# Kernel optimization log

Measured on AMD Instinct MI355X. Metric: run time of the kernel, lower is better.

## Reference

```python
import jax, jax.numpy as jnp
import numpy as np

D_MODEL = 1024
NUM_HEADS = 16
D_K = D_MODEL // NUM_HEADS


def setup_inputs() -> dict:
    key = jax.random.key(0)
    ks = jax.random.split(key, 11)
    B, S = 2, 2048
    scale = 1.0 / np.sqrt(D_MODEL)
    inp = {
        "Q": jax.random.normal(ks[0], (B, S, D_MODEL), jnp.float32),
        "K": jax.random.normal(ks[1], (B, S, D_MODEL), jnp.float32),
        "V": jax.random.normal(ks[2], (B, S, D_MODEL), jnp.float32),
        "W_q": jax.random.normal(ks[3], (D_MODEL, D_MODEL), jnp.float32) * scale,
        "b_q": jnp.zeros((D_MODEL,), jnp.float32),
        "W_k": jax.random.normal(ks[4], (D_MODEL, D_MODEL), jnp.float32) * scale,
        "b_k": jnp.zeros((D_MODEL,), jnp.float32),
        "W_v": jax.random.normal(ks[5], (D_MODEL, D_MODEL), jnp.float32) * scale,
        "b_v": jnp.zeros((D_MODEL,), jnp.float32),
        "W_o": jax.random.normal(ks[6], (D_MODEL, D_MODEL), jnp.float32) * scale,
        "b_o": jnp.zeros((D_MODEL,), jnp.float32),
    }
    return inp


def _split_heads(x):
    # [B, S, D] -> [B, H, S, d_k]
    B, S, _ = x.shape
    return x.reshape(B, S, NUM_HEADS, D_K).transpose(0, 2, 1, 3)


def reference(Q, K, V, W_q, b_q, W_k, b_k, W_v, b_v, W_o, b_o):
    # linear projections (torch Linear: x @ W.T + b)
    q = _split_heads(Q @ W_q.T + b_q)
    k = _split_heads(K @ W_k.T + b_k)
    v = _split_heads(V @ W_v.T + b_v)
    # scaled dot-product attention, full [B,H,S,S] scores as in source
    scores = jnp.einsum("bhqd,bhkd->bhqk", q, k) / jnp.sqrt(jnp.float32(D_K))
    probs = jax.nn.softmax(scores, axis=-1)
    ctx = jnp.einsum("bhqk,bhkd->bhqd", probs, v)
    # combine heads: [B,H,S,d_k] -> [B,S,D]
    B, H, S, d = ctx.shape
    ctx = ctx.transpose(0, 2, 1, 3).reshape(B, S, H * d)
    return ctx @ W_o.T + b_o
```

## Files before the change

kernel.cpp:

```cpp
#include <hip/hip_runtime.h>
#include <hip/hip_bf16.h>

typedef unsigned short u16;
typedef unsigned int u32;
typedef short s16x8 __attribute__((ext_vector_type(8)));
typedef float f32x4 __attribute__((ext_vector_type(4)));
typedef float f32x16 __attribute__((ext_vector_type(16)));
typedef u32 u32x4 __attribute__((ext_vector_type(4)));

#define DEV static __device__ __forceinline__

DEV u16 bf16_rne(float f) {
  u32 u = __builtin_bit_cast(u32, f);
  u += 0x7fffu + ((u >> 16) & 1u);
  return (u16)(u >> 16);
}

DEV u32 pack2_bf16(float a, float b) {
  u32 ua = __builtin_bit_cast(u32, a);
  u32 ub = __builtin_bit_cast(u32, b);
  ua += 0x7fffu + ((ua >> 16) & 1u);
  ub += 0x7fffu + ((ub >> 16) & 1u);
  return (ua >> 16) | (ub & 0xffff0000u);
}

#define GLDS16(g, l)                                                           \
  __builtin_amdgcn_global_load_lds(                                           \
      (const __attribute__((address_space(1))) void*)(g),                     \
      (__attribute__((address_space(3))) void*)(l), 16, 0, 0)

__global__ void cvt4_kernel(const float* s0, const float* s1, const float* s2,
                            const float* s3, u16* d0, u16* d1, u16* d2,
                            u16* d3, int n4) {
  const int z = blockIdx.y;
  const float* s = (z == 0) ? s0 : (z == 1) ? s1 : (z == 2) ? s2 : s3;
  u16* d = (z == 0) ? d0 : (z == 1) ? d1 : (z == 2) ? d2 : d3;
  int i = blockIdx.x * blockDim.x + threadIdx.x;
  if (i < n4) {
    float4 v = reinterpret_cast<const float4*>(s)[i];
    ushort4 o;
    o.x = bf16_rne(v.x);
    o.y = bf16_rne(v.y);
    o.z = bf16_rne(v.z);
    o.w = bf16_rne(v.w);
    reinterpret_cast<ushort4*>(d)[i] = o;
  }
}

__global__ __launch_bounds__(256, 3) void gemm_qkv(
    const float* __restrict__ A0, const float* __restrict__ A1,
    const float* __restrict__ A2, const u16* __restrict__ W0,
    const u16* __restrict__ W1, const u16* __restrict__ W2,
    const float* __restrict__ bias0, const float* __restrict__ bias1,
    const float* __restrict__ bias2, u16* __restrict__ C0,
    u16* __restrict__ C1v, u16* __restrict__ C2, int M, int N, int K) {
  const int z = blockIdx.z;
  const float* A = (z == 0) ? A0 : (z == 1) ? A1 : A2;
  const u16* W = (z == 0) ? W0 : (z == 1) ? W1 : W2;
  const float* bias = (z == 0) ? bias0 : (z == 1) ? bias1 : bias2;
  u16* Cout = (z == 0) ? C0 : (z == 1) ? C1v : C2;
  const float escale = (z == 0) ? 0.125f * 1.44269504088896f : 1.0f;

  __shared__ __align__(16) u16 As[128 * 64];
  __shared__ __align__(16) u16 Ws[128 * 64];
  const int tid = threadIdx.x;
  const int lane = tid & 63;
  const int w = tid >> 6;
  const int wr = w >> 1, wc = w & 1;
  const int l15 = lane & 15, l4 = lane >> 4;
  const int m0 = blockIdx.x * 128, n0 = blockIdx.y * 128;

  f32x4 acc[4][4] = {};
  float bv[4];
#pragma unroll
  for (int fc = 0; fc < 4; ++fc) bv[fc] = bias[n0 + wc * 64 + fc * 16 + l15];

  float4 pre[4][2];
  auto loadA = [&](int kt) {
#pragma unroll
    for (int i = 0; i < 4; ++i) {
      const int ch = i * 256 + tid;
      const float* s = A + (size_t)(m0 + (ch >> 3)) * K + kt + (ch & 7) * 8;
      pre[i][0] = *(const float4*)s;
      pre[i][1] = *(const float4*)(s + 4);
    }
  };
  loadA(0);

  for (int kt = 0; kt < K; kt += 64) {
    __syncthreads();
#pragma unroll
    for (int i = 0; i < 4; ++i) {
      const int ch = i * 256 + tid;
      const int row = ch >> 3, cg = ch & 7;
      u32x4 o;
      o[0] = pack2_bf16(pre[i][0].x, pre[i][0].y);
      o[1] = pack2_bf16(pre[i][0].z, pre[i][0].w);
      o[2] = pack2_bf16(pre[i][1].x, pre[i][1].y);
      o[3] = pack2_bf16(pre[i][1].z, pre[i][1].w);
      *(u32x4*)(As + (size_t)(row * 8 + (cg ^ (row & 7))) * 8) = o;
    }
#pragma unroll
    for (int i = 0; i < 4; ++i) {
      const int ch = i * 256 + tid;
      const int row = ch >> 3, cl = ch & 7;
      GLDS16(W + (size_t)(n0 + row) * K + kt + ((cl ^ (row & 7)) * 8),
             Ws + (size_t)(i * 256 + w * 64) * 8);
    }
    __syncthreads();
    if (kt + 64 < K) loadA(kt + 64);
#pragma unroll
    for (int ks = 0; ks < 2; ++ks) {
      const int sw = (ks * 4 + l4) ^ (l15 & 7);
      s16x8 a[4], b[4];
#pragma unroll
      for (int f = 0; f < 4; ++f)
        a[f] = *(const s16x8*)(As + (size_t)((wr * 64 + f * 16 + l15) * 8 + sw) * 8);
#pragma unroll
      for (int f = 0; f < 4; ++f)
        b[f] = *(const s16x8*)(Ws + (size_t)((wc * 64 + f * 16 + l15) * 8 + sw) * 8);
#pragma unroll
      for (int fr = 0; fr < 4; ++fr)
#pragma unroll
        for (int fc = 0; fc < 4; ++fc)
          acc[fr][fc] = __builtin_amdgcn_mfma_f32_16x16x32_bf16(
              a[fr], b[fc], acc[fr][fc], 0, 0, 0);
    }
  }

  if (z == 2) {
#pragma unroll
    for (int fr = 0; fr < 4; ++fr) {
      const int m = m0 + wr * 64 + fr * 16 + l4 * 4;
      const int bb = m >> 11, s = m & 2047;
#pragma unroll
      for (int fc = 0; fc < 4; ++fc) {
        const int n = n0 + wc * 64 + fc * 16 + l15;
        const int hh = n >> 6, dd = n & 63;
        ushort4 o;
        o.x = bf16_rne(acc[fr][fc][0] + bv[fc]);
        o.y = bf16_rne(acc[fr][fc][1] + bv[fc]);
        o.z = bf16_rne(acc[fr][fc][2] + bv[fc]);
        o.w = bf16_rne(acc[fr][fc][3] + bv[fc]);
        *(ushort4*)(Cout + (((size_t)(bb * 16 + hh) * 64 + dd) * 2048 + s)) = o;
      }
    }
  } else {
#pragma unroll
    for (int fr = 0; fr < 4; ++fr) {
      const int mrow = m0 + wr * 64 + fr * 16 + l4 * 4;
#pragma unroll
      for (int fc = 0; fc < 4; ++fc) {
        const int ncol = n0 + wc * 64 + fc * 16 + l15;
#pragma unroll
        for (int r = 0; r < 4; ++r)
          Cout[(size_t)(mrow + r) * N + ncol] =
              bf16_rne((acc[fr][fc][r] + bv[fc]) * escale);
      }
    }
  }
}

__global__ __launch_bounds__(256, 4) void gemm_o(
    const u16* __restrict__ A, const u16* __restrict__ W,
    const float* __restrict__ bias, float* __restrict__ Cout, int M, int N,
    int K) {
  __shared__ __align__(16) u16 As[128 * 64];
  __shared__ __align__(16) u16 Ws[64 * 64];
  const int tid = threadIdx.x;
  const int lane = tid & 63;
  const int w = tid >> 6;
  const int wr = w >> 1, wc = w & 1;
  const int l15 = lane & 15, l4 = lane >> 4;
  const int m0 = blockIdx.x * 128, n0 = blockIdx.y * 64;

  f32x4 acc[4][2] = {};
  float bv[2];
#pragma unroll
  for (int fc = 0; fc < 2; ++fc) bv[fc] = bias[n0 + wc * 32 + fc * 16 + l15];

  for (int kt = 0; kt < K; kt += 64) {
    __syncthreads();
#pragma unroll
    for (int i = 0; i < 4; ++i) {
      const int ch = i * 256 + tid;
      const int row = ch >> 3, cl = ch & 7;
      GLDS16(A + (size_t)(m0 + row) * K + kt + ((cl ^ (row & 7)) * 8),
             As + (size_t)(i * 256 + w * 64) * 8);
    }
#pragma unroll
    for (int i = 0; i < 2; ++i) {
      const int ch = i * 256 + tid;
      const int row = ch >> 3, cl = ch & 7;
      GLDS16(W + (size_t)(n0 + row) * K + kt + ((cl ^ (row & 7)) * 8),
             Ws + (size_t)(i * 256 + w * 64) * 8);
    }
    __syncthreads();
#pragma unroll
    for (int ks = 0; ks < 2; ++ks) {
      const int sw = (ks * 4 + l4) ^ (l15 & 7);
      s16x8 a[4], b[2];
#pragma unroll
      for (int f = 0; f < 4; ++f)
        a[f] = *(const s16x8*)(As + (size_t)((wr * 64 + f * 16 + l15) * 8 + sw) * 8);
#pragma unroll
      for (int f = 0; f < 2; ++f)
        b[f] = *(const s16x8*)(Ws + (size_t)((wc * 32 + f * 16 + l15) * 8 + sw) * 8);
#pragma unroll
      for (int fr = 0; fr < 4; ++fr)
#pragma unroll
        for (int fc = 0; fc < 2; ++fc)
          acc[fr][fc] = __builtin_amdgcn_mfma_f32_16x16x32_bf16(
              a[fr], b[fc], acc[fr][fc], 0, 0, 0);
    }
  }

#pragma unroll
  for (int fr = 0; fr < 4; ++fr) {
    const int mrow = m0 + wr * 64 + fr * 16 + l4 * 4;
#pragma unroll
    for (int fc = 0; fc < 2; ++fc) {
      const int ncol = n0 + wc * 32 + fc * 16 + l15;
#pragma unroll
      for (int r = 0; r < 4; ++r)
        Cout[(size_t)(mrow + r) * N + ncol] = acc[fr][fc][r] + bv[fc];
    }
  }
}

__global__ __launch_bounds__(512, 4) void attn_fused(
    const u16* __restrict__ qp, const u16* __restrict__ kp,
    const u16* __restrict__ vt, u16* __restrict__ ctx) {
  const int S = 2048, D = 1024;
  const int bh = blockIdx.x;
  const int qt = blockIdx.y;
  const int tid = threadIdx.x, lane = tid & 63, w = tid >> 6;
  const int l31 = lane & 31, l5 = lane >> 5;
  const int g = tid >> 8;
  const int tl = tid & 255;
  const int wl = tl >> 6;
  const int wq = w & 3;

  __shared__ __align__(16) u16 SM[32768];

  const size_t qkbase = ((size_t)(bh >> 4) * S) * D + (size_t)(bh & 15) * 64;
  const size_t vbase = (size_t)bh * 64 * S;

  const int q = qt * 128 + wq * 32 + l31;
  s16x8 qf[4];
#pragma unroll
  for (int ks = 0; ks < 4; ++ks)
    qf[ks] = *(const s16x8*)(qp + qkbase + (size_t)q * D + ks * 16 + l5 * 8);

  u32x4 onesw;
  onesw[0] = onesw[1] = onesw[2] = onesw[3] = 0x3F803F80u;
  const s16x8 ones = __builtin_bit_cast(s16x8, onesw);

  f32x16 octx[2] = {};
  f32x16 lacc = {};

  auto stage = [&](int buf, int ti) {
    const int kv0 = (g * 16 + ti) * 64;
    u16* Kd = SM + g * 16384 + buf * 4096;
    u16* Vd = SM + g * 16384 + 8192 + buf * 4096;
#pragma unroll
    for (int i = 0; i < 2; ++i) {
      const int gch = i * 256 + tl;
      const int kv = gch >> 3, cc = gch & 7;
      GLDS16(kp + qkbase + (size_t)(kv0 + kv) * D + ((cc ^ (kv & 7)) << 3),
             Kd + (size_t)(i * 256 + wl * 64) * 8);
    }
#pragma unroll
    for (int i = 0; i < 2; ++i) {
      const int gch = i * 256 + tl;
      const int d = gch >> 3, cc = gch & 7;
      GLDS16(vt + vbase + (size_t)d * S + kv0 + ((cc ^ (d & 7)) << 3),
             Vd + (size_t)(i * 256 + wl * 64) * 8);
    }
  };

  stage(0, 0);
  const int NT = 16;
  for (int t = 0; t < NT; ++t) {
    __syncthreads();
    if (t + 1 < NT) stage((t + 1) & 1, t + 1);
    const u16* Kb = SM + g * 16384 + (t & 1) * 4096;
    const u16* Vb = SM + g * 16384 + 8192 + (t & 1) * 4096;

    f32x16 sc[2] = {};
#pragma unroll
    for (int ks = 0; ks < 4; ++ks) {
      __builtin_amdgcn_s_setprio(1);
#pragma unroll
      for (int fk = 0; fk < 2; ++fk) {
        const int kv = fk * 32 + l31;
        const int c = (ks << 1) + l5;
        const s16x8 kf =
            *(const s16x8*)(Kb + (size_t)(kv * 8 + (c ^ (kv & 7))) * 8);
        sc[fk] = __builtin_amdgcn_mfma_f32_32x32x16_bf16(kf, qf[ks], sc[fk],
                                                         0, 0, 0);
      }
      __builtin_amdgcn_s_setprio(0);
    }

#pragma unroll
    for (int c4 = 0; c4 < 4; ++c4) {
      const int fk = c4 >> 1, hf = c4 & 1;
      float p[8];
#pragma unroll
      for (int j = 0; j < 8; ++j)
        p[j] = __builtin_amdgcn_exp2f(sc[fk][hf * 8 + j]);
      u32 x0, x1, y0, y1;
      asm("v_cvt_pk_bf16_f32 %0, %1, %2" : "=v"(x0) : "v"(p[0]), "v"(p[1]));
      asm("v_cvt_pk_bf16_f32 %0, %1, %2" : "=v"(x1) : "v"(p[2]), "v"(p[3]));
      asm("v_cvt_pk_bf16_f32 %0, %1, %2" : "=v"(y0) : "v"(p[4]), "v"(p[5]));
      asm("v_cvt_pk_bf16_f32 %0, %1, %2" : "=v"(y1) : "v"(p[6]), "v"(p[7]));
      asm("v_permlane32_swap_b32 %0, %1" : "+v"(x0), "+v"(y0));
      asm("v_permlane32_swap_b32 %0, %1" : "+v"(x1), "+v"(y1));
      u32x4 bw;
      bw[0] = x0; bw[1] = x1; bw[2] = y0; bw[3] = y1;
      const s16x8 pb = __builtin_bit_cast(s16x8, bw);
      __builtin_amdgcn_s_setprio(1);
      lacc = __builtin_amdgcn_mfma_f32_32x32x16_bf16(ones, pb, lacc, 0, 0, 0);
#pragma unroll
      for (int fd = 0; fd < 2; ++fd) {
        const int d = fd * 32 + l31;
        const int c = (c4 << 1) + l5;
        const s16x8 vf =
            *(const s16x8*)(Vb + (size_t)(d * 8 + (c ^ (d & 7))) * 8);
        octx[fd] = __builtin_amdgcn_mfma_f32_32x32x16_bf16(vf, pb, octx[fd],
                                                           0, 0, 0);
      }
      __builtin_amdgcn_s_setprio(0);
    }
  }

  const float lpart = lacc[0];

  __syncthreads();
  float* scr = (float*)(void*)SM;
  if (g == 1) {
    float* dst = scr + ((size_t)wq * 64 + lane) * 33;
#pragma unroll
    for (int fd = 0; fd < 2; ++fd)
#pragma unroll
      for (int r = 0; r < 16; ++r) dst[fd * 16 + r] = octx[fd][r];
    dst[32] = lpart;
  }
  __syncthreads();
  if (g == 0) {
    const float* src = scr + ((size_t)wq * 64 + lane) * 33;
    const float linv = 1.f / (lpart + src[32]);
#pragma unroll
    for (int fd = 0; fd < 2; ++fd)
#pragma unroll
      for (int gg = 0; gg < 4; ++gg) {
        ushort4 o;
        o.x = bf16_rne((octx[fd][gg * 4 + 0] + src[fd * 16 + gg * 4 + 0]) * linv);
        o.y = bf16_rne((octx[fd][gg * 4 + 1] + src[fd * 16 + gg * 4 + 1]) * linv);
        o.z = bf16_rne((octx[fd][gg * 4 + 2] + src[fd * 16 + gg * 4 + 2]) * linv);
        o.w = bf16_rne((octx[fd][gg * 4 + 3] + src[fd * 16 + gg * 4 + 3]) * linv);
        *(ushort4*)(ctx + qkbase + (size_t)q * D + fd * 32 + gg * 8 + l5 * 4) =
            o;
      }
  }
}

extern "C" void kernel_launch(void* const* d_in, const int* in_sizes, int n_in,
                              void* d_out, int out_size, void* d_ws,
                              size_t ws_size, hipStream_t stream) {
  (void)in_sizes; (void)n_in; (void)out_size; (void)ws_size;
  const float* Q = (const float*)d_in[0];
  const float* K = (const float*)d_in[1];
  const float* V = (const float*)d_in[2];
  const float* Wq = (const float*)d_in[3];
  const float* bq = (const float*)d_in[4];
  const float* Wk = (const float*)d_in[5];
  const float* bk = (const float*)d_in[6];
  const float* Wv = (const float*)d_in[7];
  const float* bv = (const float*)d_in[8];
  const float* Wo = (const float*)d_in[9];
  const float* bo = (const float*)d_in[10];

  const int B = 2, S = 2048, D = 1024, H = 16;
  const int M = B * S;
  const size_t NE = (size_t)M * D;
  const size_t WE = (size_t)D * D;

  u16* qp = (u16*)d_ws;
  u16* kp = qp + NE;
  u16* vtb = kp + NE;
  u16* ctxb = vtb + NE;
  u16* Wqb = ctxb + NE;
  u16* Wkb = Wqb + WE;
  u16* Wvb = Wkb + WE;
  u16* Wob = Wvb + WE;

  const int w4 = (int)(WE / 4), wb = (w4 + 255) / 256;
  cvt4_kernel<<<dim3(wb, 4), 256, 0, stream>>>(Wq, Wk, Wv, Wo, Wqb, Wkb, Wvb,
                                               Wob, w4);

  dim3 gg(M / 128, D / 128, 3);
  gemm_qkv<<<gg, 256, 0, stream>>>(Q, K, V, Wqb, Wkb, Wvb, bq, bk, bv, qp, kp,
                                   vtb, M, D, D);

  dim3 ga(B * H, S / 128);
  attn_fused<<<ga, 512, 0, stream>>>(qp, kp, vtb, ctxb);

  dim3 go(M / 128, D / 64);
  gemm_o<<<go, 256, 0, stream>>>(ctxb, Wob, bo, (float*)d_out, M, D, D);
}
```

Before: 105.3 us.

## Software-pipeline QKV GEMM with double-buffered weight tiles and two-deep A prefetch

Restructures the QKV projection GEMM main loop into a software pipeline: weight tiles are double-buffered in LDS via direct global-to-LDS loads issued one step ahead, and fp32 activation tiles are prefetched two steps ahead into alternating register sets. It waits with explicit vmcnt/lgkmcnt counts and s_barrier plus sched_barrier fences instead of __syncthreads, and fully unrolls the K loop assuming K=1024. The goal is to hide global load latency behind MFMA work. In exchange it uses more LDS and registers, which may lower occupancy under launch_bounds(256,3), and it hardcodes K and the vmcnt value.

```diff
diff --git a/kernel.cpp b/kernel.cpp
--- a/kernel.cpp
+++ b/kernel.cpp
@@ -62,71 +62,100 @@
   const float escale = (z == 0) ? 0.125f * 1.44269504088896f : 1.0f;
 
   __shared__ __align__(16) u16 As[128 * 64];
-  __shared__ __align__(16) u16 Ws[128 * 64];
+  __shared__ __align__(16) u16 Ws[2][128 * 64];
   const int tid = threadIdx.x;
   const int lane = tid & 63;
   const int w = tid >> 6;
-  const int wr = w >> 1, wc = w & 1;
+  const int wr = w >> 1, wcol = w & 1;
   const int l15 = lane & 15, l4 = lane >> 4;
   const int m0 = blockIdx.x * 128, n0 = blockIdx.y * 128;
 
   f32x4 acc[4][4] = {};
   float bv[4];
 #pragma unroll
-  for (int fc = 0; fc < 4; ++fc) bv[fc] = bias[n0 + wc * 64 + fc * 16 + l15];
-
-  float4 pre[4][2];
-  auto loadA = [&](int kt) {
-#pragma unroll
-    for (int i = 0; i < 4; ++i) {
-      const int ch = i * 256 + tid;
-      const float* s = A + (size_t)(m0 + (ch >> 3)) * K + kt + (ch & 7) * 8;
-      pre[i][0] = *(const float4*)s;
-      pre[i][1] = *(const float4*)(s + 4);
-    }
-  };
-  loadA(0);
-
-  for (int kt = 0; kt < K; kt += 64) {
-    __syncthreads();
-#pragma unroll
-    for (int i = 0; i < 4; ++i) {
-      const int ch = i * 256 + tid;
-      const int row = ch >> 3, cg = ch & 7;
-      u32x4 o;
-      o[0] = pack2_bf16(pre[i][0].x, pre[i][0].y);
-      o[1] = pack2_bf16(pre[i][0].z, pre[i][0].w);
-      o[2] = pack2_bf16(pre[i][1].x, pre[i][1].y);
-      o[3] = pack2_bf16(pre[i][1].z, pre[i][1].w);
-      *(u32x4*)(As + (size_t)(row * 8 + (cg ^ (row & 7))) * 8) = o;
-    }
-#pragma unroll
-    for (int i = 0; i < 4; ++i) {
-      const int ch = i * 256 + tid;
-      const int row = ch >> 3, cl = ch & 7;
-      GLDS16(W + (size_t)(n0 + row) * K + kt + ((cl ^ (row & 7)) * 8),
-             Ws + (size_t)(i * 256 + w * 64) * 8);
-    }
-    __syncthreads();
-    if (kt + 64 < K) loadA(kt + 64);
-#pragma unroll
-    for (int ks = 0; ks < 2; ++ks) {
-      const int sw = (ks * 4 + l4) ^ (l15 & 7);
-      s16x8 a[4], b[4];
-#pragma unroll
-      for (int f = 0; f < 4; ++f)
-        a[f] = *(const s16x8*)(As + (size_t)((wr * 64 + f * 16 + l15) * 8 + sw) * 8);
-#pragma unroll
-      for (int f = 0; f < 4; ++f)
-        b[f] = *(const s16x8*)(Ws + (size_t)((wc * 64 + f * 16 + l15) * 8 + sw) * 8);
-#pragma unroll
-      for (int fr = 0; fr < 4; ++fr)
-#pragma unroll
-        for (int fc = 0; fc < 4; ++fc)
-          acc[fr][fc] = __builtin_amdgcn_mfma_f32_16x16x32_bf16(
-              a[fr], b[fc], acc[fr][fc], 0, 0, 0);
-    }
-  }
+  for (int fc = 0; fc < 4; ++fc) bv[fc] = bias[n0 + wcol * 64 + fc * 16 + l15];
+
+  float4 pA0[4][2], pA1[4][2];
+
+#define LOADA(kt, P)                                                           \
+  {                                                                            \
+    _Pragma("unroll") for (int i = 0; i < 4; ++i) {                            \
+      const int ch = i * 256 + tid;                                            \
+      const float* sA = A + (size_t)(m0 + (ch >> 3)) * K + (kt) + (ch & 7) * 8;\
+      P[i][0] = *(const float4*)sA;                                            \
+      P[i][1] = *(const float4*)(sA + 4);                                      \
+    }                                                                          \
+  }
+#define GLDSW(kt, bufi)                                                        \
+  {                                                                            \
+    _Pragma("unroll") for (int i = 0; i < 4; ++i) {                            \
+      const int ch = i * 256 + tid;                                            \
+      const int row = ch >> 3, cl = ch & 7;                                    \
+      GLDS16(W + (size_t)(n0 + row) * K + (kt) + ((cl ^ (row & 7)) * 8),       \
+             &Ws[bufi][(size_t)(i * 256 + w * 64) * 8]);                       \
+    }                                                                          \
+  }
+#define CVTA(P)                                                                \
+  {                                                                            \
+    _Pragma("unroll") for (int i = 0; i < 4; ++i) {                            \
+      const int ch = i * 256 + tid;                                            \
+      const int row = ch >> 3, cg = ch & 7;                                    \
+      u32x4 o;                                                                 \
+      o[0] = pack2_bf16(P[i][0].x, P[i][0].y);                                 \
+      o[1] = pack2_bf16(P[i][0].z, P[i][0].w);                                 \
+      o[2] = pack2_bf16(P[i][1].x, P[i][1].y);                                 \
+      o[3] = pack2_bf16(P[i][1].z, P[i][1].w);                                 \
+      *(u32x4*)(As + (size_t)(row * 8 + (cg ^ (row & 7))) * 8) = o;            \
+    }                                                                          \
+  }
+#define COMPUTE(bufi)                                                          \
+  {                                                                            \
+    _Pragma("unroll") for (int ks = 0; ks < 2; ++ks) {                         \
+      const int sw = (ks * 4 + l4) ^ (l15 & 7);                                \
+      s16x8 a[4], b[4];                                                        \
+      _Pragma("unroll") for (int f = 0; f < 4; ++f) a[f] =                     \
+          *(const s16x8*)(As + (size_t)((wr * 64 + f * 16 + l15) * 8 + sw) * 8);\
+      _Pragma("unroll") for (int f = 0; f < 4; ++f) b[f] =                     \
+          *(const s16x8*)(&Ws[bufi][0] +                                       \
+                          (size_t)((wcol * 64 + f * 16 + l15) * 8 + sw) * 8);  \
+      _Pragma("unroll") for (int fr = 0; fr < 4; ++fr)                         \
+          _Pragma("unroll") for (int fc = 0; fc < 4; ++fc) acc[fr][fc] =       \
+              __builtin_amdgcn_mfma_f32_16x16x32_bf16(a[fr], b[fc],            \
+                                                      acc[fr][fc], 0, 0, 0);   \
+    }                                                                          \
+  }
+
+  LOADA(0, pA0);
+  GLDSW(0, 0);
+  LOADA(64, pA1);
+  CVTA(pA0);
+
+#define ITER(t, WC, WN, PL, PC)                                                \
+  {                                                                            \
+    GLDSW((((t) + 1) & 15) * 64, WN);                                          \
+    LOADA((((t) + 2) & 15) * 64, PL);                                          \
+    asm volatile("s_waitcnt vmcnt(20)" ::: "memory");         \
+    __builtin_amdgcn_sched_barrier(0);                                         \
+    asm volatile("s_waitcnt lgkmcnt(0)" ::: "memory");     \
+    __builtin_amdgcn_sched_barrier(0);                                         \
+    __builtin_amdgcn_s_barrier();                   \
+    __builtin_amdgcn_sched_barrier(0);                                         \
+    COMPUTE(WC);                                                               \
+    __builtin_amdgcn_sched_barrier(0);                                         \
+    __builtin_amdgcn_s_barrier();                     \
+    __builtin_amdgcn_sched_barrier(0);                                         \
+    if ((t) < 15) CVTA(PC);                            \
+  }
+
+  for (int tt = 0; tt < 8; ++tt) {
+    ITER(2 * tt, 0, 1, pA0, pA1);
+    ITER(2 * tt + 1, 1, 0, pA1, pA0);
+  }
+#undef ITER
+#undef COMPUTE
+#undef CVTA
+#undef GLDSW
+#undef LOADA
 
   if (z == 2) {
 #pragma unroll
@@ -135,7 +164,7 @@
       const int bb = m >> 11, s = m & 2047;
 #pragma unroll
       for (int fc = 0; fc < 4; ++fc) {
-        const int n = n0 + wc * 64 + fc * 16 + l15;
+        const int n = n0 + wcol * 64 + fc * 16 + l15;
         const int hh = n >> 6, dd = n & 63;
         ushort4 o;
         o.x = bf16_rne(acc[fr][fc][0] + bv[fc]);
@@ -151,7 +180,7 @@
       const int mrow = m0 + wr * 64 + fr * 16 + l4 * 4;
 #pragma unroll
       for (int fc = 0; fc < 4; ++fc) {
-        const int ncol = n0 + wc * 64 + fc * 16 + l15;
+        const int ncol = n0 + wcol * 64 + fc * 16 + l15;
 #pragma unroll
         for (int r = 0; r < 4; ++r)
           Cout[(size_t)(mrow + r) * N + ncol] =
```

Result: slower. 128.1 us (+21.6%).

## Pre-convert Q/K/V inputs to bf16 and load A tiles via global_load_lds

Applied to the files above, without the earlier changes.

Adds a separate conversion pass that turns the fp32 Q, K and V activations into bf16 buffers. The QKV GEMM then streams A tiles directly into LDS with global_load_lds instead of loading fp32 into registers, packing and writing them. The GEMM tile is also narrowed from 128x128 to 128x64 with a higher occupancy bound, and the Q bf16 buffer is reused to hold the attention context. This removes register pressure and in-loop conversion work, at the cost of an extra kernel launch and an extra full read and write of the activations.

```diff
diff --git a/kernel.cpp b/kernel.cpp
--- a/kernel.cpp
+++ b/kernel.cpp
@@ -14,14 +14,6 @@
   u32 u = __builtin_bit_cast(u32, f);
   u += 0x7fffu + ((u >> 16) & 1u);
   return (u16)(u >> 16);
-}
-
-DEV u32 pack2_bf16(float a, float b) {
-  u32 ua = __builtin_bit_cast(u32, a);
-  u32 ub = __builtin_bit_cast(u32, b);
-  ua += 0x7fffu + ((ua >> 16) & 1u);
-  ub += 0x7fffu + ((ub >> 16) & 1u);
-  return (ua >> 16) | (ub & 0xffff0000u);
 }
 
 #define GLDS16(g, l)                                                           \
@@ -47,82 +39,65 @@
   }
 }
 
-__global__ __launch_bounds__(256, 3) void gemm_qkv(
-    const float* __restrict__ A0, const float* __restrict__ A1,
-    const float* __restrict__ A2, const u16* __restrict__ W0,
+__global__ __launch_bounds__(256, 5) void gemm_qkv(
+    const u16* __restrict__ A0, const u16* __restrict__ A1,
+    const u16* __restrict__ A2, const u16* __restrict__ W0,
     const u16* __restrict__ W1, const u16* __restrict__ W2,
     const float* __restrict__ bias0, const float* __restrict__ bias1,
     const float* __restrict__ bias2, u16* __restrict__ C0,
     u16* __restrict__ C1v, u16* __restrict__ C2, int M, int N, int K) {
   const int z = blockIdx.z;
-  const float* A = (z == 0) ? A0 : (z == 1) ? A1 : A2;
+  const u16* A = (z == 0) ? A0 : (z == 1) ? A1 : A2;
   const u16* W = (z == 0) ? W0 : (z == 1) ? W1 : W2;
   const float* bias = (z == 0) ? bias0 : (z == 1) ? bias1 : bias2;
   u16* Cout = (z == 0) ? C0 : (z == 1) ? C1v : C2;
   const float escale = (z == 0) ? 0.125f * 1.44269504088896f : 1.0f;
 
   __shared__ __align__(16) u16 As[128 * 64];
-  __shared__ __align__(16) u16 Ws[128 * 64];
+  __shared__ __align__(16) u16 Ws[64 * 64];
   const int tid = threadIdx.x;
   const int lane = tid & 63;
   const int w = tid >> 6;
   const int wr = w >> 1, wc = w & 1;
   const int l15 = lane & 15, l4 = lane >> 4;
-  const int m0 = blockIdx.x * 128, n0 = blockIdx.y * 128;
-
-  f32x4 acc[4][4] = {};
-  float bv[4];
-#pragma unroll
-  for (int fc = 0; fc < 4; ++fc) bv[fc] = bias[n0 + wc * 64 + fc * 16 + l15];
-
-  float4 pre[4][2];
-  auto loadA = [&](int kt) {
+  const int m0 = blockIdx.x * 128, n0 = blockIdx.y * 64;
+
+  f32x4 acc[4][2] = {};
+  float bv[2];
+#pragma unroll
+  for (int fc = 0; fc < 2; ++fc) bv[fc] = bias[n0 + wc * 32 + fc * 16 + l15];
+
+  for (int kt = 0; kt < K; kt += 64) {
+    __syncthreads();
 #pragma unroll
     for (int i = 0; i < 4; ++i) {
       const int ch = i * 256 + tid;
-      const float* s = A + (size_t)(m0 + (ch >> 3)) * K + kt + (ch & 7) * 8;
-      pre[i][0] = *(const float4*)s;
-      pre[i][1] = *(const float4*)(s + 4);
-    }
-  };
-  loadA(0);
-
-  for (int kt = 0; kt < K; kt += 64) {
-    __syncthreads();
-#pragma unroll
-    for (int i = 0; i < 4; ++i) {
-      const int ch = i * 256 + tid;
-      const int row = ch >> 3, cg = ch & 7;
-      u32x4 o;
-      o[0] = pack2_bf16(pre[i][0].x, pre[i][0].y);
-      o[1] = pack2_bf16(pre[i][0].z, pre[i][0].w);
-      o[2] = pack2_bf16(pre[i][1].x, pre[i][1].y);
-      o[3] = pack2_bf16(pre[i][1].z, pre[i][1].w);
-      *(u32x4*)(As + (size_t)(row * 8 + (cg ^ (row & 7))) * 8) = o;
-    }
-#pragma unroll
-    for (int i = 0; i < 4; ++i) {
+      const int row = ch >> 3, cl = ch & 7;
+      GLDS16(A + (size_t)(m0 + row) * K + kt + ((cl ^ (row & 7)) * 8),
+             As + (size_t)(i * 256 + w * 64) * 8);
+    }
+#pragma unroll
+    for (int i = 0; i < 2; ++i) {
       const int ch = i * 256 + tid;
       const int row = ch >> 3, cl = ch & 7;
       GLDS16(W + (size_t)(n0 + row) * K + kt + ((cl ^ (row & 7)) * 8),
              Ws + (size_t)(i * 256 + w * 64) * 8);
     }
     __syncthreads();
-    if (kt + 64 < K) loadA(kt + 64);
 #pragma unroll
     for (int ks = 0; ks < 2; ++ks) {
       const int sw = (ks * 4 + l4) ^ (l15 & 7);
-      s16x8 a[4], b[4];
+      s16x8 a[4], b[2];
 #pragma unroll
       for (int f = 0; f < 4; ++f)
         a[f] = *(const s16x8*)(As + (size_t)((wr * 64 + f * 16 + l15) * 8 + sw) * 8);
 #pragma unroll
-      for (int f = 0; f < 4; ++f)
-        b[f] = *(const s16x8*)(Ws + (size_t)((wc * 64 + f * 16 + l15) * 8 + sw) * 8);
+      for (int f = 0; f < 2; ++f)
+        b[f] = *(const s16x8*)(Ws + (size_t)((wc * 32 + f * 16 + l15) * 8 + sw) * 8);
 #pragma unroll
       for (int fr = 0; fr < 4; ++fr)
 #pragma unroll
-        for (int fc = 0; fc < 4; ++fc)
+        for (int fc = 0; fc < 2; ++fc)
           acc[fr][fc] = __builtin_amdgcn_mfma_f32_16x16x32_bf16(
               a[fr], b[fc], acc[fr][fc], 0, 0, 0);
     }
@@ -134,8 +109,8 @@
       const int m = m0 + wr * 64 + fr * 16 + l4 * 4;
       const int bb = m >> 11, s = m & 2047;
 #pragma unroll
-      for (int fc = 0; fc < 4; ++fc) {
-        const int n = n0 + wc * 64 + fc * 16 + l15;
+      for (int fc = 0; fc < 2; ++fc) {
+        const int n = n0 + wc * 32 + fc * 16 + l15;
         const int hh = n >> 6, dd = n & 63;
         ushort4 o;
         o.x = bf16_rne(acc[fr][fc][0] + bv[fc]);
@@ -150,8 +125,8 @@
     for (int fr = 0; fr < 4; ++fr) {
       const int mrow = m0 + wr * 64 + fr * 16 + l4 * 4;
 #pragma unroll
-      for (int fc = 0; fc < 4; ++fc) {
-        const int ncol = n0 + wc * 64 + fc * 16 + l15;
+      for (int fc = 0; fc < 2; ++fc) {
+        const int ncol = n0 + wc * 32 + fc * 16 + l15;
 #pragma unroll
         for (int r = 0; r < 4; ++r)
           Cout[(size_t)(mrow + r) * N + ncol] =
@@ -387,26 +362,31 @@
   const size_t NE = (size_t)M * D;
   const size_t WE = (size_t)D * D;
 
-  u16* qp = (u16*)d_ws;
+  u16* Qb = (u16*)d_ws;
+  u16* Kb = Qb + NE;
+  u16* Vb = Kb + NE;
+  u16* qp = Vb + NE;
   u16* kp = qp + NE;
   u16* vtb = kp + NE;
-  u16* ctxb = vtb + NE;
-  u16* Wqb = ctxb + NE;
+  u16* Wqb = vtb + NE;
   u16* Wkb = Wqb + WE;
   u16* Wvb = Wkb + WE;
   u16* Wob = Wvb + WE;
 
+  const int n4 = (int)(NE / 4), nb = (n4 + 255) / 256;
   const int w4 = (int)(WE / 4), wb = (w4 + 255) / 256;
+  cvt4_kernel<<<dim3(nb, 3), 256, 0, stream>>>(Q, K, V, nullptr, Qb, Kb, Vb,
+                                               nullptr, n4);
   cvt4_kernel<<<dim3(wb, 4), 256, 0, stream>>>(Wq, Wk, Wv, Wo, Wqb, Wkb, Wvb,
                                                Wob, w4);
 
-  dim3 gg(M / 128, D / 128, 3);
-  gemm_qkv<<<gg, 256, 0, stream>>>(Q, K, V, Wqb, Wkb, Wvb, bq, bk, bv, qp, kp,
-                                   vtb, M, D, D);
+  dim3 gg(M / 128, D / 64, 3);
+  gemm_qkv<<<gg, 256, 0, stream>>>(Qb, Kb, Vb, Wqb, Wkb, Wvb, bq, bk, bv, qp,
+                                   kp, vtb, M, D, D);
 
   dim3 ga(B * H, S / 128);
-  attn_fused<<<ga, 512, 0, stream>>>(qp, kp, vtb, ctxb);
+  attn_fused<<<ga, 512, 0, stream>>>(qp, kp, vtb, Qb);
 
   dim3 go(M / 128, D / 64);
-  gemm_o<<<go, 256, 0, stream>>>(ctxb, Wob, bo, (float*)d_out, M, D, D);
-}
+  gemm_o<<<go, 256, 0, stream>>>(Qb, Wob, bo, (float*)d_out, M, D, D);
+}
```

After: 112.1 us. 6.4% more time.
